# Optimization experiments

Hardware: AMD Instinct MI355X
Metric: run time of the kernel (lower is better)

## Reference

```python
import jax, jax.numpy as jnp
import numpy as np


def _count_components(img, cls):
    """Count 4-connected components of pixels equal to `cls` in a 2D int map.

    Equivalent to the numba DFS flood fill: each component is counted once.
    Implemented as min-label propagation: seed every in-class pixel with its
    linear index, iterate min over 4-neighbors (same-class only, since
    out-of-class pixels hold the sentinel BIG) until convergence; a component
    root is a pixel whose final label equals its own index.
    """
    H, W = img.shape
    BIG = H * W  # sentinel larger than any pixel index
    mask = img == cls
    idx = jnp.arange(BIG, dtype=jnp.int32).reshape(H, W)
    lab0 = jnp.where(mask, idx, BIG).astype(jnp.int32)

    def cond(state):
        return state[1]

    def body(state):
        lab, _ = state
        p = jnp.pad(lab, 1, constant_values=BIG)
        nmin = jnp.minimum(jnp.minimum(p[:-2, 1:-1], p[2:, 1:-1]),
                           jnp.minimum(p[1:-1, :-2], p[1:-1, 2:]))
        new = jnp.where(mask, jnp.minimum(lab, nmin), BIG)
        return new, jnp.any(new != lab)

    lab, _ = jax.lax.while_loop(cond, body, (lab0, jnp.array(True)))
    # roots: in-class pixels whose propagated label is their own index
    return jnp.sum(mask & (lab == idx)).astype(jnp.float32)


def _counts23(img):
    # component counts for labels 2 and 3 (the only ones the loss uses)
    return _count_components(img, 2), _count_components(img, 3)


def setup_inputs() -> dict:
    key = jax.random.key(0)
    k1, k2 = jax.random.split(key)
    pred = jax.random.normal(k1, (8, 4, 1, 768, 768), dtype=jnp.float32)
    anno = jax.random.randint(k2, (8, 1, 768, 768), 0, 4, dtype=jnp.int32)
    return {"pred": pred, "anno": anno}


def reference(pred, anno):
    # pred: [B, C, 1, H, W], anno: [B, 1, H, W]
    pred_argmax = jnp.argmax(pred, axis=1)[:, 0]  # [B, H, W] (detached semantics)
    anno_map = anno[:, 0]                          # [B, H, W]
    a2, a3 = jax.vmap(_counts23)(anno_map)
    p2, p3 = jax.vmap(_counts23)(pred_argmax)
    term2 = 1.0 - 2.0 * jnp.minimum(p2, a2) / (a2 + p2)
    term3 = 1.0 - 2.0 * jnp.minimum(p3, a3) / (a3 + p3)
    # original sums per-batch terms into connEF, then loss = connEF / 2
    return jnp.sum(term2 + term3) / 2.0
```

## Files before the change

kernel.cpp:

```cpp
#include <hip/hip_runtime.h>

#define W     768
#define PIX   (768*768)
#define NMAPS 16
#define TROWS 6
#define TPX   (TROWS*W)
#define NT    (768/TROWS)
#define NB    (NT-1)
#define NSEG  (TPX/64)
#define NIT   (NSEG/4)
#define CSLOT 16


__device__ __forceinline__ int find_root_p(volatile int* L, int x) {
    int y = L[x] >> 2;
    while (y != x) { x = y; y = L[x] >> 2; }
    return x;
}

__device__ __forceinline__ void unite_p(int* L, int a, int b, int c) {
    volatile int* Lv = L;
    while (true) {
        a = find_root_p(Lv, a);
        b = find_root_p(Lv, b);
        if (a == b) return;
        if (a > b) { int t = a; a = b; b = t; }
        int old = atomicMin(&L[b], (a << 2) | c);
        if ((old >> 2) == b) return;
        b = old >> 2;
    }
}

__device__ __forceinline__ bool unite_gp(int* L, int a, int b, int c) {
    volatile int* Lv = L;
    while (true) {
        a = find_root_p(Lv, a);
        b = find_root_p(Lv, b);
        if (a == b) return false;
        if (a > b) { int t = a; a = b; b = t; }
        int old = atomicMin(&L[b], (a << 2) | c);
        if ((old >> 2) == b) return true;
        b = old >> 2;
    }
}


__global__ void zero_counts_k(int* counts) {
    int i = blockIdx.x * 256 + threadIdx.x;
    if (i < 32 * CSLOT) counts[i] = 0;
}

__global__ __launch_bounds__(256) void fused_k(const float* __restrict__ pred,
                                               const int*   __restrict__ anno,
                                               int* __restrict__ labels,
                                               int* __restrict__ counts, int m0) {
    __shared__ int lab[TPX];
    __shared__ int s2[4], s3[4];

    int mc   = blockIdx.x / NT;
    int t    = blockIdx.x - mc * NT;
    int m    = m0 + mc;
    int tid  = threadIdx.x;
    int wid  = tid >> 6;
    int lane = tid & 63;

    unsigned long long cpack = 0;
    int pc[3] = {0, 0, 0};
    int pm[3] = {0, 0, 0};

    const int*   asrc = anno + (size_t)m * PIX + (size_t)t * TPX;
    const float* psrc = pred + (size_t)(m < 8 ? 0 : (m - 8)) * 4 * PIX + (size_t)t * TPX;
    bool is_anno = (m < 8);

    #pragma unroll
    for (int it = 0; it < NIT; ++it) {
        int seg = wid + 4 * it;
        int px  = seg * 64 + lane;
        int c;
        if (is_anno) {
            c = asrc[px] & 3;
        } else {
            float v0 = psrc[px];
            float v1 = psrc[(size_t)PIX + px];
            float v2 = psrc[(size_t)2 * PIX + px];
            float v3 = psrc[(size_t)3 * PIX + px];
            c = 0; float bv = v0;
            if (v1 > bv) { bv = v1; c = 1; }
            if (v2 > bv) { bv = v2; c = 2; }
            if (v3 > bv) { bv = v3; c = 3; }
        }
        cpack |= (unsigned long long)c << (2 * it);
        int cl = __shfl_up(c, 1);
        unsigned long long bm = __ballot(lane == 0 || c != cl);
        int ms = 63 - __clzll(bm & ((2ULL << lane) - 1));
        lab[px] = ((seg * 64 + ms) << 2) | c;
        asm volatile("s_waitcnt lgkmcnt(0)" ::: "memory");
        const int sl = it % 3;
        if (it >= 3) {
            if ((c & 2) && c == pc[sl]) {
                int mx = ms > pm[sl] ? ms : pm[sl];
                if (lane == mx) unite_p(lab, px - W, px, c);
            }
        }
        pc[sl] = c; pm[sl] = ms;
    }
    __syncthreads();

    if (tid < TROWS * 11) {
        int row = tid / 11, j = tid % 11;
        int px  = row * W + (j + 1) * 64;
        int v = lab[px], c = v & 3;
        if (c & 2) {
            int vl = lab[px - 1];
            if ((vl & 3) == c) unite_p(lab, px - 1, px, c);
        }
    }
    __syncthreads();

    int c2 = 0, c3 = 0;
    int lbase = t * TPX;
    int* gl = labels + (size_t)mc * PIX + lbase;
    for (int it = 0; it < NIT; ++it) {
        int seg = wid + 4 * it;
        int px  = seg * 64 + lane;
        int c   = (int)((cpack >> (2 * it)) & 3);
        int outv;
        if (c & 2) {
            int r = find_root_p(lab, px);
            if (r == px) { if (c == 2) c2++; else c3++; }
            outv = ((lbase + r) << 2) | c;
        } else {
            outv = ((lbase + px) << 2) | c;
        }
        gl[px] = outv;
    }
    for (int off = 32; off; off >>= 1) {
        c2 += __shfl_down(c2, off, 64);
        c3 += __shfl_down(c3, off, 64);
    }
    if (lane == 0) { s2[wid] = c2; s3[wid] = c3; }
    __syncthreads();
    if (tid == 0) {
        int t2 = s2[0] + s2[1] + s2[2] + s2[3];
        int t3 = s3[0] + s3[1] + s3[2] + s3[3];
        if (t2) atomicAdd(&counts[(m * 2 + 0) * CSLOT], t2);
        if (t3) atomicAdd(&counts[(m * 2 + 1) * CSLOT], t3);
    }
}

__global__ __launch_bounds__(256) void boundary_k(int* __restrict__ labels,
                                                  int* __restrict__ counts, int m0) {
    __shared__ int s2[4], s3[4];
    const int PERMAP = NB * W;
    int gid = blockIdx.x * 256 + threadIdx.x;
    int mc  = gid / PERMAP;
    int i   = gid - mc * PERMAP;
    int b   = i / W;
    int col = i - b * W;
    int m   = m0 + mc;
    int lane = threadIdx.x & 63;

    int* L = labels + (size_t)mc * PIX;
    int p1 = b * TPX + (TROWS - 1) * W + col;
    int p2 = p1 + W;

    int m2 = 0, m3 = 0;
    int v1 = L[p1], v2 = L[p2];
    int c1 = v1 & 3, c2_ = v2 & 3;
    int pv1 = __shfl_up(v1, 1), pv2 = __shfl_up(v2, 1);
    bool match = (c1 == c2_) && (c1 & 2);
    bool redundant = (lane > 0) && (pv1 == v1) && (pv2 == v2);
    if (match && !redundant) {
        if (unite_gp(L, p1, p2, c1)) { if (c1 == 2) m2++; else m3++; }
    }
    for (int off = 32; off; off >>= 1) {
        m2 += __shfl_down(m2, off, 64);
        m3 += __shfl_down(m3, off, 64);
    }
    int wid = threadIdx.x >> 6;
    if (lane == 0) { s2[wid] = m2; s3[wid] = m3; }
    __syncthreads();
    if (threadIdx.x == 0) {
        int t2 = s2[0] + s2[1] + s2[2] + s2[3];
        int t3 = s3[0] + s3[1] + s3[2] + s3[3];
        if (t2) atomicSub(&counts[(m * 2 + 0) * CSLOT], t2);
        if (t3) atomicSub(&counts[(m * 2 + 1) * CSLOT], t3);
    }
}

__global__ void final_k(const int* __restrict__ counts, float* __restrict__ out) {
    float s = 0.0f;
    for (int b = 0; b < 8; ++b) {
        float a2 = (float)counts[(b * 2 + 0) * CSLOT];
        float a3 = (float)counts[(b * 2 + 1) * CSLOT];
        float p2 = (float)counts[((8 + b) * 2 + 0) * CSLOT];
        float p3 = (float)counts[((8 + b) * 2 + 1) * CSLOT];
        float t2 = 1.0f - 2.0f * fminf(p2, a2) / (a2 + p2);
        float t3 = 1.0f - 2.0f * fminf(p3, a3) / (a3 + p3);
        s += t2 + t3;
    }
    out[0] = 0.5f * s;
}


extern "C" void kernel_launch(void* const* d_in, const int* in_sizes, int n_in,
                              void* d_out, int out_size, void* d_ws, size_t ws_size,
                              hipStream_t stream) {
    const float* pred = (const float*)d_in[0];
    const int*   anno = (const int*)d_in[1];
    float* out = (float*)d_out;

    int* counts = (int*)d_ws;
    char* base  = (char*)d_ws + 4096;

    const size_t per_map = (size_t)PIX * 4;
    size_t avail = (ws_size > 4096) ? ws_size - 4096 : 0;
    int K = (int)(avail / per_map);
    if (K > NMAPS) K = NMAPS;
    if (K < 1)     K = 1;

    zero_counts_k<<<2, 256, 0, stream>>>(counts);

    for (int m0 = 0; m0 < NMAPS; m0 += K) {
        int nm = NMAPS - m0; if (nm > K) nm = K;
        int* labels = (int*)base;
        fused_k   <<<dim3(nm * NT), 256, 0, stream>>>(pred, anno, labels, counts, m0);
        boundary_k<<<dim3(nm * (NB * W / 256)), 256, 0, stream>>>(labels, counts, m0);
    }
    final_k<<<1, 1, 0, stream>>>(counts, out);
}
```

Before: 69.69 us.

## Write only tile-edge rows and roots to global labels; vectorize boundary merge

The final pass of fused_k now counts roots straight from the shared label word, with no find, and writes full resolved labels only for the first and last rows of each tile. Interior pixels are written only when they are roots, which is all the global union-find in boundary_k needs. This cuts global write traffic and find work. boundary_k now handles two columns per thread with int2 loads and a 2D grid. The zeroing kernel becomes hipMemsetAsync, the cpack register and the explicit LDS waitcnt are removed, and correctness now relies on boundary merges touching only edge rows and roots.

```diff
diff --git a/kernel.cpp b/kernel.cpp
--- a/kernel.cpp
+++ b/kernel.cpp
@@ -45,11 +45,6 @@
 }
 
 
-__global__ void zero_counts_k(int* counts) {
-    int i = blockIdx.x * 256 + threadIdx.x;
-    if (i < 32 * CSLOT) counts[i] = 0;
-}
-
 __global__ __launch_bounds__(256) void fused_k(const float* __restrict__ pred,
                                                const int*   __restrict__ anno,
                                                int* __restrict__ labels,
@@ -64,7 +59,6 @@
     int wid  = tid >> 6;
     int lane = tid & 63;
 
-    unsigned long long cpack = 0;
     int pc[3] = {0, 0, 0};
     int pm[3] = {0, 0, 0};
 
@@ -89,12 +83,10 @@
             if (v2 > bv) { bv = v2; c = 2; }
             if (v3 > bv) { bv = v3; c = 3; }
         }
-        cpack |= (unsigned long long)c << (2 * it);
         int cl = __shfl_up(c, 1);
         unsigned long long bm = __ballot(lane == 0 || c != cl);
         int ms = 63 - __clzll(bm & ((2ULL << lane) - 1));
         lab[px] = ((seg * 64 + ms) << 2) | c;
-        asm volatile("s_waitcnt lgkmcnt(0)" ::: "memory");
         const int sl = it % 3;
         if (it >= 3) {
             if ((c & 2) && c == pc[sl]) {
@@ -120,19 +112,27 @@
     int c2 = 0, c3 = 0;
     int lbase = t * TPX;
     int* gl = labels + (size_t)mc * PIX + lbase;
+    #pragma unroll
     for (int it = 0; it < NIT; ++it) {
         int seg = wid + 4 * it;
         int px  = seg * 64 + lane;
-        int c   = (int)((cpack >> (2 * it)) & 3);
-        int outv;
-        if (c & 2) {
-            int r = find_root_p(lab, px);
-            if (r == px) { if (c == 2) c2++; else c3++; }
-            outv = ((lbase + r) << 2) | c;
-        } else {
-            outv = ((lbase + px) << 2) | c;
-        }
-        gl[px] = outv;
+        int v   = lab[px];
+        int c   = v & 3;
+        bool incls  = (c & 2) != 0;
+        bool isroot = incls && ((v >> 2) == px);
+        if (isroot) { if (c == 2) c2++; else c3++; }
+        if (it < 3 || it >= NIT - 3) {
+            int outv;
+            if (incls) {
+                int r = find_root_p(lab, px);
+                outv = ((lbase + r) << 2) | c;
+            } else {
+                outv = ((lbase + px) << 2) | c;
+            }
+            gl[px] = outv;
+        } else if (isroot) {
+            gl[px] = ((lbase + px) << 2) | c;
+        }
     }
     for (int off = 32; off; off >>= 1) {
         c2 += __shfl_down(c2, off, 64);
@@ -151,27 +151,32 @@
 __global__ __launch_bounds__(256) void boundary_k(int* __restrict__ labels,
                                                   int* __restrict__ counts, int m0) {
     __shared__ int s2[4], s3[4];
-    const int PERMAP = NB * W;
-    int gid = blockIdx.x * 256 + threadIdx.x;
-    int mc  = gid / PERMAP;
-    int i   = gid - mc * PERMAP;
-    int b   = i / W;
-    int col = i - b * W;
-    int m   = m0 + mc;
+    const int HM = NB * (W / 2);
+    int i    = blockIdx.x * 256 + threadIdx.x;
+    int mc   = blockIdx.y;
+    int m    = m0 + mc;
     int lane = threadIdx.x & 63;
 
-    int* L = labels + (size_t)mc * PIX;
-    int p1 = b * TPX + (TROWS - 1) * W + col;
-    int p2 = p1 + W;
-
     int m2 = 0, m3 = 0;
-    int v1 = L[p1], v2 = L[p2];
-    int c1 = v1 & 3, c2_ = v2 & 3;
-    int pv1 = __shfl_up(v1, 1), pv2 = __shfl_up(v2, 1);
-    bool match = (c1 == c2_) && (c1 & 2);
-    bool redundant = (lane > 0) && (pv1 == v1) && (pv2 == v2);
-    if (match && !redundant) {
-        if (unite_gp(L, p1, p2, c1)) { if (c1 == 2) m2++; else m3++; }
+    if (i < HM) {
+        int b   = i / (W / 2);
+        int col = (i - b * (W / 2)) * 2;
+        int* L  = labels + (size_t)mc * PIX;
+        int p1  = b * TPX + (TROWS - 1) * W + col;
+        int p2  = p1 + W;
+        int2 va = *(const int2*)&L[p1];
+        int2 vb = *(const int2*)&L[p2];
+        int pay = __shfl_up(va.y, 1), pby = __shfl_up(vb.y, 1);
+        int c0 = va.x & 3;
+        if (c0 == (vb.x & 3) && (c0 & 2)) {
+            bool red = (lane > 0) && (pay == va.x) && (pby == vb.x);
+            if (!red && unite_gp(L, p1, p2, c0)) { if (c0 == 2) m2++; else m3++; }
+        }
+        int c1 = va.y & 3;
+        if (c1 == (vb.y & 3) && (c1 & 2)) {
+            bool red = (va.x == va.y) && (vb.x == vb.y);
+            if (!red && unite_gp(L, p1 + 1, p2 + 1, c1)) { if (c1 == 2) m2++; else m3++; }
+        }
     }
     for (int off = 32; off; off >>= 1) {
         m2 += __shfl_down(m2, off, 64);
@@ -219,13 +224,14 @@
     if (K > NMAPS) K = NMAPS;
     if (K < 1)     K = 1;
 
-    zero_counts_k<<<2, 256, 0, stream>>>(counts);
-
+    hipMemsetAsync(counts, 0, 32 * CSLOT * sizeof(int), stream);
+
+    const int HM = NB * (W / 2);
     for (int m0 = 0; m0 < NMAPS; m0 += K) {
         int nm = NMAPS - m0; if (nm > K) nm = K;
         int* labels = (int*)base;
         fused_k   <<<dim3(nm * NT), 256, 0, stream>>>(pred, anno, labels, counts, m0);
-        boundary_k<<<dim3(nm * (NB * W / 256)), 256, 0, stream>>>(labels, counts, m0);
+        boundary_k<<<dim3((HM + 255) / 256, nm), 256, 0, stream>>>(labels, counts, m0);
     }
     final_k<<<1, 1, 0, stream>>>(counts, out);
 }
```

After: 59.01 us. 1.18x faster.
